# Kernel tuning notes

Measured on AMD Instinct MI355X. Metric: run time of the kernel, lower is better.

## Reference

```python
import jax, jax.numpy as jnp
import numpy as np

KERNELS = (2, 3, 6, 7)
ALPHA = 2.0
DT = 1.0  # time=1.0, step_size=1.0 -> one RK4 (3/8 rule) step, as torchdiffeq 'rk4'


def _conv(x, w, b):
    # x: [B,C,N,L], w: [O,I,1,k] -> valid conv over time axis
    y = jax.lax.conv_general_dilated(x, w, (1, 1), 'VALID',
                                     dimension_numbers=('NCHW', 'OIHW', 'NCHW'))
    return y + b[None, :, None, None]


def _inception(x, ws, bs):
    outs = [_conv(x, w, b) for w, b in zip(ws, bs)]
    L = outs[-1].shape[-1]  # shortest output (largest kernel=7)
    return jnp.concatenate([o[..., -L:] for o in outs], axis=1)


def _norm_adj(adj):
    A = adj + jnp.eye(adj.shape[0], dtype=adj.dtype)
    dinv = A.sum(1) ** -0.5
    return dinv[:, None] * A * dinv[None, :]  # D^-1/2 (A+I) D^-1/2


def _cgp(x, A_norm, mw, mb):
    f = lambda y: 0.5 * ALPHA * (jnp.einsum('ncwl,vw->ncvl', y, A_norm) - y)
    k1 = f(x)
    y2 = x + (DT / 3.0) * k1
    k2 = f(y2)
    y3 = x + DT * (k2 - k1 / 3.0)
    k3 = f(y3)
    y4 = x + DT * (k1 - k2 + k3)
    k4 = f(y4)
    yf = x + (DT / 8.0) * (k1 + 3.0 * (k2 + k3) + k4)
    # odefunc.out collects the state at each of the 4 f-evals, plus final state
    cat = jnp.concatenate([x, y2, y3, y4, yf], axis=1)  # [B, 5C, N, L]
    return _conv(cat, mw, mb)


def setup_inputs() -> dict:
    key = jax.random.key(0)
    B, C, N, T = 8, 64, 512, 64
    cq = C // 4
    ks = jax.random.split(key, 24)
    d = {
        'x': jax.random.normal(ks[0], (B, C, N, T), dtype=jnp.float32),
        'adj': jax.random.uniform(ks[1], (N, N), dtype=jnp.float32),
    }
    i = 2
    for branch in ('i1', 'i2'):
        for j, k in enumerate(KERNELS):
            d[f'{branch}w{j}'] = 0.1 * jax.random.normal(ks[i], (cq, C, 1, k), dtype=jnp.float32); i += 1
            d[f'{branch}b{j}'] = 0.1 * jax.random.normal(ks[i], (cq,), dtype=jnp.float32); i += 1
    d['m1w'] = 0.1 * jax.random.normal(ks[i], (C, 5 * C, 1, 1), dtype=jnp.float32); i += 1
    d['m1b'] = 0.1 * jax.random.normal(ks[i], (C,), dtype=jnp.float32); i += 1
    d['m2w'] = 0.1 * jax.random.normal(ks[i], (C, 5 * C, 1, 1), dtype=jnp.float32); i += 1
    d['m2b'] = 0.1 * jax.random.normal(ks[i], (C,), dtype=jnp.float32)
    return d


def reference(x, adj,
              i1w0, i1b0, i1w1, i1b1, i1w2, i1b2, i1w3, i1b3,
              i2w0, i2b0, i2w1, i2b1, i2w2, i2b2, i2w3, i2b3,
              m1w, m1b, m2w, m2b):
    T = x.shape[-1]  # receptive_field
    filt = jnp.tanh(_inception(x, (i1w0, i1w1, i1w2, i1w3), (i1b0, i1b1, i1b2, i1b3)))
    gate = jax.nn.sigmoid(_inception(x, (i2w0, i2w1, i2w2, i2w3), (i2b0, i2b1, i2b2, i2b3)))
    h = filt * gate  # dropout is identity in eval mode
    An = _norm_adj(adj)
    AnT = _norm_adj(adj.T)
    h = _cgp(h, An, m1w, m1b) + _cgp(h, AnT, m2w, m2b)
    pad = T - h.shape[-1]
    return jnp.pad(h, ((0, 0), (0, 0), (0, 0), (pad, 0)))
```

## Files before the change

kernel.cpp:

```cpp
#include <hip/hip_runtime.h>
#include <math.h>

#define NN 512
#define BB 8
#define CC 64
#define TT 64
#define LL 58
#define CL (CC*LL)
#define BCL (BB*CC*LL)
#define SZ ((size_t)NN*BCL)

typedef _Float16 half8 __attribute__((ext_vector_type(8)));
typedef _Float16 half4 __attribute__((ext_vector_type(4)));
typedef float f32x4 __attribute__((ext_vector_type(4)));

__global__ __launch_bounds__(64) void prep_adj(const float* __restrict__ adj,
                                               float* __restrict__ dinv1,
                                               float* __restrict__ dinv2){
  int v = blockIdx.x;
  int lane = threadIdx.x;
  float rs = 0.f, cs = 0.f;
  for (int w = lane; w < NN; w += 64){
    rs += adj[v*NN + w];
    cs += adj[w*NN + v];
  }
  for (int off = 32; off > 0; off >>= 1){
    rs += __shfl_down(rs, off);
    cs += __shfl_down(cs, off);
  }
  if (lane == 0){
    dinv1[v] = 1.f / sqrtf(rs + 1.f);
    dinv2[v] = 1.f / sqrtf(cs + 1.f);
  }
}

__global__ __launch_bounds__(256) void build_norm(const float* __restrict__ adj,
                                                  const float* __restrict__ dinv1,
                                                  const float* __restrict__ dinv2,
                                                  _Float16* __restrict__ An,
                                                  _Float16* __restrict__ AnT){
  int v = blockIdx.x;
  float d1v = dinv1[v], d2v = dinv2[v];
  for (int w = threadIdx.x; w < NN; w += 256){
    float diag = (v == w) ? 1.f : 0.f;
    An[v*NN + w]  = (_Float16)(d1v * (adj[v*NN + w] + diag) * dinv1[w] - diag);
    AnT[v*NN + w] = (_Float16)(d2v * (adj[w*NN + v] + diag) * dinv2[w] - diag);
  }
}

__global__ __launch_bounds__(256) void u_prep(const float* __restrict__ W1,
                                              const float* __restrict__ W2,
                                              _Float16* __restrict__ U1,
                                              _Float16* __restrict__ U2){
  const float coef[5][5] = {
    {1.f, 1.f, 1.f, 1.f, 1.f},
    {0.f, 1.f/3.f, 2.f/3.f, 1.f, 1.f},
    {0.f, 0.f, 1.f/3.f, 1.f/3.f, 0.5f},
    {0.f, 0.f, 0.f, 1.f/3.f, 1.f/6.f},
    {0.f, 0.f, 0.f, 0.f, 1.f/24.f}};
  int idx = blockIdx.x*256 + threadIdx.x;
  int o = idx / 320, rem = idx - o*320;
  int d = rem >> 6, c = rem & 63;
  float a1 = 0.f, a2 = 0.f;
  #pragma unroll
  for (int s = 0; s < 5; ++s){
    float cf = coef[d][s];
    a1 += cf * W1[o*320 + s*64 + c];
    a2 += cf * W2[o*320 + s*64 + c];
  }
  U1[idx] = (_Float16)a1;
  U2[idx] = (_Float16)a2;
}

__global__ __launch_bounds__(448) void wfg_prep(
    const float* __restrict__ w10, const float* __restrict__ w11,
    const float* __restrict__ w12, const float* __restrict__ w13,
    const float* __restrict__ w20, const float* __restrict__ w21,
    const float* __restrict__ w22, const float* __restrict__ w23,
    const float* __restrict__ b10, const float* __restrict__ b11,
    const float* __restrict__ b12, const float* __restrict__ b13,
    const float* __restrict__ b20, const float* __restrict__ b21,
    const float* __restrict__ b22, const float* __restrict__ b23,
    _Float16* __restrict__ WfG, float* __restrict__ biasFG){
  int r = blockIdx.x;
  int t = threadIdx.x;
  int qp = t >> 6, ic = t & 63;
  int gate = r >> 6;
  int j = (r >> 4) & 3;
  int oc = r & 15;
  const int kjs[4] = {2, 3, 6, 7};
  int kj = kjs[j];
  const float* wsel = gate ? ((j==0)?w20:(j==1)?w21:(j==2)?w22:w23)
                           : ((j==0)?w10:(j==1)?w11:(j==2)?w12:w13);
  int off = 7 - kj;
  float val = (qp >= off) ? wsel[(oc*64 + ic)*kj + (qp - off)] : 0.f;
  WfG[(size_t)r*448 + t] = (_Float16)val;
  if (t == 0){
    const float* bsel = gate ? ((j==0)?b20:(j==1)?b21:(j==2)?b22:b23)
                             : ((j==0)?b10:(j==1)?b11:(j==2)?b12:b13);
    biasFG[r] = bsel[oc];
  }
}

__global__ __launch_bounds__(256) void xt_prep(const float* __restrict__ x,
                                               _Float16* __restrict__ xTg){
  __shared__ float T[64][65];
  int n = blockIdx.x;
  int b = blockIdx.y;
  int tid = threadIdx.x;
  #pragma unroll
  for (int r = 0; r < 4; ++r){
    int f = tid + r*256;
    int ic = f >> 4, t4 = f & 15;
    float4 v = *(const float4*)&x[(((size_t)(b*64 + ic))*512 + n)*64 + t4*4];
    T[ic][t4*4+0] = v.x; T[ic][t4*4+1] = v.y;
    T[ic][t4*4+2] = v.z; T[ic][t4*4+3] = v.w;
  }
  __syncthreads();
  #pragma unroll
  for (int r = 0; r < 2; ++r){
    int f = tid + r*256;
    int t = f >> 3, ch = f & 7;
    half8 hv;
    #pragma unroll
    for (int q2 = 0; q2 < 8; ++q2) hv[q2] = (_Float16)T[ch*8 + q2][t];
    *(half8*)&xTg[(((size_t)(b*64 + t))*512 + n)*64 + ch*8] = hv;
  }
}

__global__ __launch_bounds__(256, 3) void inception_mfma(
    const _Float16* __restrict__ xTg,
    const _Float16* __restrict__ WfG,
    const float* __restrict__ biasFG,
    _Float16* __restrict__ S_h){
  __shared__ _Float16 X[13*32*64];
  int nt = blockIdx.x;
  int lt = blockIdx.y;
  int b  = blockIdx.z;
  int n0 = nt*32, l0 = lt*7;
  int tid = threadIdx.x;

  int sch = tid & 7, sn = (tid >> 3) & 31;
  #pragma unroll
  for (int r = 0; r < 13; ++r){
    int t = l0 + r;
    half8 v = {};
    if (t < 64)
      v = *(const half8*)&xTg[(((size_t)(b*64 + t))*512 + n0 + sn)*64 + sch*8];
    *(half8*)&X[(size_t)(r*256 + sn*8 + (sch ^ (sn & 7)))*8] = v;
  }

  int w = tid >> 6, lane = tid & 63;
  int m = lane & 15, kg = lane >> 4;

  half8 wF[14], wG[14];
  const _Float16* wb = WfG + (size_t)(w*16 + m)*448 + kg*8;
  #pragma unroll
  for (int s = 0; s < 14; ++s){
    wF[s] = *(const half8*)(wb + s*32);
    wG[s] = *(const half8*)(wb + (size_t)64*448 + s*32);
  }
  f32x4 bF = *(const f32x4*)&biasFG[w*16 + kg*4];
  f32x4 bG = *(const f32x4*)&biasFG[64 + w*16 + kg*4];

  __syncthreads();

  for (int ll = 0; ll < 7; ++ll){
    f32x4 aF0 = {}, aF1 = {}, aG0 = {}, aG1 = {};
    #pragma unroll
    for (int s = 0; s < 14; ++s){
      int t = ll + (s >> 1);
      int c0 = (s & 1)*4 + kg;
      half8 b0 = *(half8*)&X[(size_t)(t*256 + m*8        + (c0 ^ (m & 7)))*8];
      half8 b1 = *(half8*)&X[(size_t)(t*256 + (16+m)*8   + (c0 ^ (m & 7)))*8];
      aF0 = __builtin_amdgcn_mfma_f32_16x16x32_f16(wF[s], b0, aF0, 0, 0, 0);
      aG0 = __builtin_amdgcn_mfma_f32_16x16x32_f16(wG[s], b0, aG0, 0, 0, 0);
      aF1 = __builtin_amdgcn_mfma_f32_16x16x32_f16(wF[s], b1, aF1, 0, 0, 0);
      aG1 = __builtin_amdgcn_mfma_f32_16x16x32_f16(wG[s], b1, aG1, 0, 0, 0);
    }
    int l = l0 + ll;
    if (l < LL){
      #pragma unroll
      for (int rr = 0; rr < 4; ++rr){
        int c = w*16 + kg*4 + rr;
        float F0 = aF0[rr] + bF[rr];
        float G0 = aG0[rr] + bG[rr];
        float F1 = aF1[rr] + bF[rr];
        float G1 = aG1[rr] + bG[rr];
        float h0 = (2.f*__builtin_amdgcn_rcpf(1.f + __expf(-2.f*F0)) - 1.f)
                 * __builtin_amdgcn_rcpf(1.f + __expf(-G0));
        float h1 = (2.f*__builtin_amdgcn_rcpf(1.f + __expf(-2.f*F1)) - 1.f)
                 * __builtin_amdgcn_rcpf(1.f + __expf(-G1));
        size_t base = ((size_t)(b*64 + c)*LL + l)*NN + n0;
        S_h[base + m]      = (_Float16)h0;
        S_h[base + 16 + m] = (_Float16)h1;
      }
    }
  }
}

__device__ __forceinline__ void gll16(const _Float16* g, _Float16* l){
  __builtin_amdgcn_global_load_lds(
      (const __attribute__((address_space(1))) unsigned int*)g,
      (__attribute__((address_space(3))) unsigned int*)l, 16, 0, 0);
}

__global__ __launch_bounds__(512, 2) void gemm_z2(
    const _Float16* __restrict__ A0, const _Float16* __restrict__ B0,
    _Float16* __restrict__ O0,
    const _Float16* __restrict__ A1, const _Float16* __restrict__ B1,
    _Float16* __restrict__ O1){
  const _Float16* __restrict__ A = blockIdx.z ? A1 : A0;
  const _Float16* __restrict__ B = blockIdx.z ? B1 : B0;
  _Float16* __restrict__ O = blockIdx.z ? O1 : O0;

  __shared__ _Float16 L[65536];

  const int m0 = blockIdx.x * 256;
  const int v0 = blockIdx.y * 256;
  const int tid = threadIdx.x;
  const int ww = tid >> 6;
  const int lane = tid & 63;
  const int lr = lane & 15;
  const int kg = lane >> 4;
  const int wv = ww >> 2;
  const int wm = ww & 3;

  const int srow = lane >> 3;
  const int schk = (lane & 7) ^ srow;
  const _Float16* gA = A + (size_t)(v0 + ww*32 + srow)*NN + schk*8;
  const _Float16* gB = B + (size_t)(m0 + ww*32 + srow)*NN + schk*8;
  _Float16* ldsA = L + ww*2048;
  _Float16* ldsB = ldsA + 16384;

  #define STAGE(buf, kt)                                                  \
    {                                                                     \
      const _Float16* ga_ = gA + (kt)*64;                                 \
      const _Float16* gb_ = gB + (kt)*64;                                 \
      _Float16* la_ = ldsA + (buf)*32768;                                 \
      _Float16* lb_ = ldsB + (buf)*32768;                                 \
      _Pragma("unroll")                                                   \
      for (int s_ = 0; s_ < 4; ++s_){                                     \
        gll16(ga_ + (size_t)s_*8*NN, la_ + s_*512);                       \
        gll16(gb_ + (size_t)s_*8*NN, lb_ + s_*512);                       \
      }                                                                   \
    }

  f32x4 acc[8][4] = {};

  STAGE(0, 0)
  STAGE(1, 1)
  asm volatile("s_waitcnt vmcnt(8)" ::: "memory");
  asm volatile("s_barrier" ::: "memory");

  const int axor = lr & 7;
  const int aBase = (wv*128 + lr)*64;
  const int bBase = (wm*64 + lr)*64;
  const int c0 = ((kg    ) ^ axor)*8;
  const int c1 = ((kg + 4) ^ axor)*8;

  for (int kt = 0; kt < 8; ++kt){
    const _Float16* la = L + (kt & 1)*32768;
    const _Float16* lb = la + 16384;
    half8 af[8], bf[4];

    #pragma unroll
    for (int i = 0; i < 8; ++i) af[i] = *(const half8*)&la[aBase + i*1024 + c0];
    #pragma unroll
    for (int j = 0; j < 4; ++j) bf[j] = *(const half8*)&lb[bBase + j*1024 + c0];
    __builtin_amdgcn_s_setprio(1);
    #pragma unroll
    for (int i = 0; i < 8; ++i)
      #pragma unroll
      for (int j = 0; j < 4; ++j)
        acc[i][j] = __builtin_amdgcn_mfma_f32_16x16x32_f16(af[i], bf[j], acc[i][j], 0, 0, 0);
    __builtin_amdgcn_s_setprio(0);

    #pragma unroll
    for (int i = 0; i < 8; ++i) af[i] = *(const half8*)&la[aBase + i*1024 + c1];
    #pragma unroll
    for (int j = 0; j < 4; ++j) bf[j] = *(const half8*)&lb[bBase + j*1024 + c1];
    asm volatile("s_waitcnt lgkmcnt(0)" ::: "memory");
    asm volatile("s_barrier" ::: "memory");

    if (kt < 6) STAGE(kt & 1, kt + 2)

    __builtin_amdgcn_s_setprio(1);
    #pragma unroll
    for (int i = 0; i < 8; ++i)
      #pragma unroll
      for (int j = 0; j < 4; ++j)
        acc[i][j] = __builtin_amdgcn_mfma_f32_16x16x32_f16(af[i], bf[j], acc[i][j], 0, 0, 0);
    __builtin_amdgcn_s_setprio(0);

    if (kt < 6){
      asm volatile("s_waitcnt vmcnt(8)" ::: "memory");
      asm volatile("s_barrier" ::: "memory");
    } else if (kt == 6){
      asm volatile("s_waitcnt vmcnt(0)" ::: "memory");
      asm volatile("s_barrier" ::: "memory");
    }
  }
  #undef STAGE

  #pragma unroll
  for (int i = 0; i < 8; ++i){
    int vrow = v0 + wv*128 + i*16 + kg*4;
    #pragma unroll
    for (int j = 0; j < 4; ++j){
      int mcol = m0 + wm*64 + j*16 + lr;
      half4 oq;
      #pragma unroll
      for (int rr = 0; rr < 4; ++rr) oq[rr] = (_Float16)acc[i][j][rr];
      *(half4*)&O[(size_t)mcol*NN + vrow] = oq;
    }
  }
}

template<int PASS>
__global__ __launch_bounds__(256) void combine_mfma(
    const _Float16* __restrict__ Sh, const _Float16* __restrict__ S2,
    const _Float16* __restrict__ S3, const _Float16* __restrict__ S4,
    const _Float16* __restrict__ Sf,
    const _Float16* __restrict__ Wc,
    const float* __restrict__ bias,
    _Float16* __restrict__ tmp){
  __shared__ _Float16 Xsh[64*258];
  __shared__ _Float16 Wsh[64*72];
  __shared__ float Bsh[64];
  int v0 = blockIdx.x * 256;
  int l  = blockIdx.y;
  int b  = blockIdx.z;
  int tid = threadIdx.x;
  int w = tid >> 6, lane = tid & 63;
  int lr = lane & 15, kg = lane >> 4;

  if (tid < 64) Bsh[tid] = bias[tid];

  const _Float16* Sarr[5] = {Sh, S2, S3, S4, Sf};
  f32x4 acc[4][4] = {};

  for (int kt = 0; kt < 5; ++kt){
    const _Float16* S = Sarr[kt];
    __syncthreads();
    #pragma unroll
    for (int r = 0; r < 8; ++r){
      int f = tid + r*256;
      int c = f >> 5, ch = f & 31;
      half8 xv = *(const half8*)&S[((size_t)(b*64 + c)*58 + l)*512 + v0 + ch*8];
      *(half8*)&Xsh[c*258 + ch*8] = xv;
    }
    #pragma unroll
    for (int r = 0; r < 2; ++r){
      int f = tid + r*256;
      int o = f >> 3, ch = f & 7;
      *(half8*)&Wsh[o*72 + ch*8] = *(const half8*)&Wc[(size_t)o*320 + kt*64 + ch*8];
    }
    __syncthreads();

    #pragma unroll
    for (int ks = 0; ks < 2; ++ks){
      int k0 = ks*32;
      half8 aW[4];
      #pragma unroll
      for (int jj = 0; jj < 4; ++jj)
        aW[jj] = *(half8*)&Wsh[(jj*16 + lr)*72 + k0 + kg*8];
      #pragma unroll
      for (int vt = 0; vt < 4; ++vt){
        half8 bX;
        #pragma unroll
        for (int j = 0; j < 8; ++j)
          bX[j] = Xsh[(k0 + kg*8 + j)*258 + w*64 + vt*16 + lr];
        #pragma unroll
        for (int jj = 0; jj < 4; ++jj)
          acc[vt][jj] = __builtin_amdgcn_mfma_f32_16x16x32_f16(aW[jj], bX, acc[vt][jj], 0, 0, 0);
      }
    }
  }

  size_t rowbase = ((size_t)b*58 + l)*64;
  #pragma unroll
  for (int jj = 0; jj < 4; ++jj){
    #pragma unroll
    for (int rr = 0; rr < 4; ++rr){
      int o = jj*16 + kg*4 + rr;
      float bv = Bsh[o];
      size_t obase = (rowbase + o)*512 + v0 + w*64 + lr;
      #pragma unroll
      for (int vt = 0; vt < 4; ++vt){
        float val = acc[vt][jj][rr] + bv;
        size_t addr = obase + vt*16;
        if (PASS == 0) tmp[addr] = (_Float16)val;
        else           tmp[addr] = (_Float16)((float)tmp[addr] + val);
      }
    }
  }
}

__global__ __launch_bounds__(256) void untranspose(const _Float16* __restrict__ tmp,
                                                   float* __restrict__ out){
  __shared__ float T[58][65];
  int o = blockIdx.x;
  int b = blockIdx.y;
  int v0 = blockIdx.z * 64;
  int t = threadIdx.x;
  for (int idx = t; idx < 58*64; idx += 256){
    int lr = idx >> 6, vv = idx & 63;
    T[lr][vv] = (float)tmp[((size_t)(b*58 + lr)*64 + o)*NN + v0 + vv];
  }
  __syncthreads();
  #pragma unroll
  for (int i = 0; i < 16; ++i){
    int c = t + i*256;
    int vv = c >> 6, tt = c & 63;
    float val = (tt < 6) ? 0.f : T[tt - 6][vv];
    out[((size_t)(b*64 + o)*NN + v0 + vv)*TT + tt] = val;
  }
}

extern "C" void kernel_launch(void* const* d_in, const int* in_sizes, int n_in,
                              void* d_out, int out_size, void* d_ws, size_t ws_size,
                              hipStream_t stream){
  const float* x   = (const float*)d_in[0];
  const float* adj = (const float*)d_in[1];
  const float* w1[4] = {(const float*)d_in[2],  (const float*)d_in[4],
                        (const float*)d_in[6],  (const float*)d_in[8]};
  const float* b1[4] = {(const float*)d_in[3],  (const float*)d_in[5],
                        (const float*)d_in[7],  (const float*)d_in[9]};
  const float* w2[4] = {(const float*)d_in[10], (const float*)d_in[12],
                        (const float*)d_in[14], (const float*)d_in[16]};
  const float* b2[4] = {(const float*)d_in[11], (const float*)d_in[13],
                        (const float*)d_in[15], (const float*)d_in[17]};
  const float* m1w = (const float*)d_in[18];
  const float* m1b = (const float*)d_in[19];
  const float* m2w = (const float*)d_in[20];
  const float* m2b = (const float*)d_in[21];

  char* wsb = (char*)d_ws;
  float* dinv1 = (float*)(wsb);
  float* dinv2 = (float*)(wsb + 2048);
  _Float16* U1  = (_Float16*)(wsb + 4096);
  _Float16* U2  = (_Float16*)(wsb + 4096 + 40960);
  _Float16* Mn  = (_Float16*)(wsb + 167936);
  _Float16* MnT = (_Float16*)(wsb + 167936 + 524288);
  size_t sbytes = SZ * 2;
  char* sbase = wsb + 1216512;
  _Float16* S_h = (_Float16*)(sbase);
  _Float16* S2  = (_Float16*)(sbase + sbytes);
  _Float16* S3  = (_Float16*)(sbase + 2*sbytes);
  _Float16* S4  = (_Float16*)(sbase + 3*sbytes);
  _Float16* S5  = (_Float16*)(sbase + 4*sbytes);
  _Float16* tmp = (_Float16*)(sbase + 5*sbytes);
  _Float16* xTg = S2;
  _Float16* WfG = (_Float16*)(sbase + 6*sbytes);
  float* biasFG = (float*)(sbase + 6*sbytes + 114688);
  _Float16* M2  = (_Float16*)(sbase + 6*sbytes + 131072);
  _Float16* MT2 = (_Float16*)(sbase + 6*sbytes + 131072 + 524288);
  float* out = (float*)d_out;

  prep_adj<<<NN, 64, 0, stream>>>(adj, dinv1, dinv2);
  build_norm<<<NN, 256, 0, stream>>>(adj, dinv1, dinv2, Mn, MnT);
  gemm_z2<<<dim3(NN/256, NN/256, 2), 512, 0, stream>>>(MnT, Mn, M2, Mn, MnT, MT2);
  u_prep<<<80, 256, 0, stream>>>(m1w, m2w, U1, U2);
  wfg_prep<<<128, 448, 0, stream>>>(
      w1[0],w1[1],w1[2],w1[3], w2[0],w2[1],w2[2],w2[3],
      b1[0],b1[1],b1[2],b1[3], b2[0],b2[1],b2[2],b2[3], WfG, biasFG);
  xt_prep<<<dim3(NN, BB), 256, 0, stream>>>(x, xTg);
  inception_mfma<<<dim3(16, 9, 8), 256, 0, stream>>>(xTg, WfG, biasFG, S_h);

  dim3 gz(BCL/256, NN/256, 2);
  dim3 gc(2, LL, BB);
  for (int pass = 0; pass < 2; ++pass){
    const _Float16* Mp  = pass ? MnT : Mn;
    const _Float16* Mp2 = pass ? MT2 : M2;
    gemm_z2<<<gz, 512, 0, stream>>>(Mp, S_h, S2, Mp2, S_h, S3);
    gemm_z2<<<gz, 512, 0, stream>>>(Mp2, S2, S4, Mp2, S3, S5);
    if (pass == 0)
      combine_mfma<0><<<gc, 256, 0, stream>>>(S_h, S2, S3, S4, S5, U1, m1b, tmp);
    else
      combine_mfma<1><<<gc, 256, 0, stream>>>(S_h, S2, S3, S4, S5, U2, m2b, tmp);
  }
  untranspose<<<dim3(64, 8, 8), 256, 0, stream>>>(tmp, out);
}
```

Measured before the change: 529.8 us.

## Restructure gemm_z2 with half-tile pipelining, XCD-aware block remap, and LDS-staged stores

The GEMM kernel now streams each 64-wide K tile in two 32-wide halves with a new LDS swizzle, interleaving global-to-LDS prefetch with MFMA groups under finer barriers. It also flattens the grid to 1D and remaps block IDs across the 8 XCDs so that blocks sharing an operand land together. The epilogue transposes results through LDS so that global stores are coalesced 16-byte writes instead of strided half4 stores. The aim is better load/compute overlap, better L2 locality and cheaper output writes. The cost is more barriers per iteration and more complex wait-count bookkeeping.

```diff
diff --git a/kernel.cpp b/kernel.cpp
--- a/kernel.cpp
+++ b/kernel.cpp
@@ -204,20 +204,30 @@
       (const __attribute__((address_space(1))) unsigned int*)g,
       (__attribute__((address_space(3))) unsigned int*)l, 16, 0, 0);
 }
+#define BAR() asm volatile("s_barrier" ::: "memory")
 
 __global__ __launch_bounds__(512, 2) void gemm_z2(
+    int nx,
     const _Float16* __restrict__ A0, const _Float16* __restrict__ B0,
     _Float16* __restrict__ O0,
     const _Float16* __restrict__ A1, const _Float16* __restrict__ B1,
     _Float16* __restrict__ O1){
-  const _Float16* __restrict__ A = blockIdx.z ? A1 : A0;
-  const _Float16* __restrict__ B = blockIdx.z ? B1 : B0;
-  _Float16* __restrict__ O = blockIdx.z ? O1 : O0;
-
   __shared__ _Float16 L[65536];
 
-  const int m0 = blockIdx.x * 256;
-  const int v0 = blockIdx.y * 256;
+  int bid = blockIdx.x;
+  int q8 = gridDim.x >> 3;
+  int virt = (bid & 7)*q8 + (bid >> 3);
+  int y = virt & 1;
+  int pair = virt >> 1;
+  int x = pair % nx;
+  int z = pair / nx;
+
+  const _Float16* __restrict__ A = z ? A1 : A0;
+  const _Float16* __restrict__ B = z ? B1 : B0;
+  _Float16* __restrict__ O = z ? O1 : O0;
+
+  const int m0 = x * 256;
+  const int v0 = y * 256;
   const int tid = threadIdx.x;
   const int ww = tid >> 6;
   const int lane = tid & 63;
@@ -226,94 +236,110 @@
   const int wv = ww >> 2;
   const int wm = ww & 3;
 
-  const int srow = lane >> 3;
-  const int schk = (lane & 7) ^ srow;
-  const _Float16* gA = A + (size_t)(v0 + ww*32 + srow)*NN + schk*8;
-  const _Float16* gB = B + (size_t)(m0 + ww*32 + srow)*NN + schk*8;
-  _Float16* ldsA = L + ww*2048;
-  _Float16* ldsB = ldsA + 16384;
-
-  #define STAGE(buf, kt)                                                  \
-    {                                                                     \
-      const _Float16* ga_ = gA + (kt)*64;                                 \
-      const _Float16* gb_ = gB + (kt)*64;                                 \
-      _Float16* la_ = ldsA + (buf)*32768;                                 \
-      _Float16* lb_ = ldsB + (buf)*32768;                                 \
-      _Pragma("unroll")                                                   \
-      for (int s_ = 0; s_ < 4; ++s_){                                     \
-        gll16(ga_ + (size_t)s_*8*NN, la_ + s_*512);                       \
-        gll16(gb_ + (size_t)s_*8*NN, lb_ + s_*512);                       \
-      }                                                                   \
-    }
-
+  const int srow = lane >> 2;
+  const int gch  = (lane & 3) ^ (srow & 3);
+  const _Float16* gAb = A + (size_t)(v0 + ww*32 + srow)*NN + gch*8;
+  const _Float16* gBb = B + (size_t)(m0 + ww*32 + srow)*NN + gch*8;
+
+  #define STAGE_A(tt, kk)                                                   \
+    { char* l_ = (char*)L + (size_t)((tt)&1)*65536 + (size_t)(kk)*16384     \
+                 + ww*2048;                                                 \
+      const _Float16* g_ = gAb + (tt)*64 + (kk)*32;                         \
+      gll16(g_,         (_Float16*)l_);                                     \
+      gll16(g_ + 16*NN, (_Float16*)(l_ + 1024)); }
+  #define STAGE_B(tt, kk)                                                   \
+    { char* l_ = (char*)L + (size_t)((tt)&1)*65536 + 32768                  \
+                 + (size_t)(kk)*16384 + ww*2048;                            \
+      const _Float16* g_ = gBb + (tt)*64 + (kk)*32;                         \
+      gll16(g_,         (_Float16*)l_);                                     \
+      gll16(g_ + 16*NN, (_Float16*)(l_ + 1024)); }
+
+  const int csw = (kg ^ (lr & 3)) * 16;
+  const int aR = (wv*128 + lr)*64 + csw;
+  const int bR = 32768 + (wm*64 + lr)*64 + csw;
+
+  half8 af[4], bf[4];
   f32x4 acc[8][4] = {};
 
-  STAGE(0, 0)
-  STAGE(1, 1)
+  #define LOADS_A(buf, kk, ih)                                              \
+    _Pragma("unroll")                                                       \
+    for (int q_ = 0; q_ < 4; ++q_)                                          \
+      af[q_] = *(const half8*)((char*)L + (buf)*65536 + (kk)*16384          \
+                               + aR + ((ih)*4 + q_)*1024);
+  #define LOADS_B(buf, kk)                                                  \
+    _Pragma("unroll")                                                       \
+    for (int q_ = 0; q_ < 4; ++q_)                                          \
+      bf[q_] = *(const half8*)((char*)L + (buf)*65536 + (kk)*16384          \
+                               + bR + q_*1024);
+  #define MFMA16(ih)                                                        \
+    __builtin_amdgcn_s_setprio(1);                                          \
+    _Pragma("unroll")                                                       \
+    for (int i_ = 0; i_ < 4; ++i_)                                          \
+      _Pragma("unroll")                                                     \
+      for (int j_ = 0; j_ < 4; ++j_)                                        \
+        acc[(ih)*4 + i_][j_] = __builtin_amdgcn_mfma_f32_16x16x32_f16(      \
+            af[i_], bf[j_], acc[(ih)*4 + i_][j_], 0, 0, 0);                 \
+    __builtin_amdgcn_s_setprio(0);
+
+  STAGE_A(0,0) STAGE_B(0,0)
+  STAGE_A(0,1) STAGE_B(0,1)
+  STAGE_A(1,0) STAGE_B(1,0)
   asm volatile("s_waitcnt vmcnt(8)" ::: "memory");
-  asm volatile("s_barrier" ::: "memory");
-
-  const int axor = lr & 7;
-  const int aBase = (wv*128 + lr)*64;
-  const int bBase = (wm*64 + lr)*64;
-  const int c0 = ((kg    ) ^ axor)*8;
-  const int c1 = ((kg + 4) ^ axor)*8;
-
+  BAR();
+
+  #pragma unroll
   for (int kt = 0; kt < 8; ++kt){
-    const _Float16* la = L + (kt & 1)*32768;
-    const _Float16* lb = la + 16384;
-    half8 af[8], bf[4];
-
-    #pragma unroll
-    for (int i = 0; i < 8; ++i) af[i] = *(const half8*)&la[aBase + i*1024 + c0];
-    #pragma unroll
-    for (int j = 0; j < 4; ++j) bf[j] = *(const half8*)&lb[bBase + j*1024 + c0];
-    __builtin_amdgcn_s_setprio(1);
-    #pragma unroll
-    for (int i = 0; i < 8; ++i)
-      #pragma unroll
-      for (int j = 0; j < 4; ++j)
-        acc[i][j] = __builtin_amdgcn_mfma_f32_16x16x32_f16(af[i], bf[j], acc[i][j], 0, 0, 0);
-    __builtin_amdgcn_s_setprio(0);
-
-    #pragma unroll
-    for (int i = 0; i < 8; ++i) af[i] = *(const half8*)&la[aBase + i*1024 + c1];
-    #pragma unroll
-    for (int j = 0; j < 4; ++j) bf[j] = *(const half8*)&lb[bBase + j*1024 + c1];
-    asm volatile("s_waitcnt lgkmcnt(0)" ::: "memory");
-    asm volatile("s_barrier" ::: "memory");
-
-    if (kt < 6) STAGE(kt & 1, kt + 2)
-
-    __builtin_amdgcn_s_setprio(1);
-    #pragma unroll
-    for (int i = 0; i < 8; ++i)
-      #pragma unroll
-      for (int j = 0; j < 4; ++j)
-        acc[i][j] = __builtin_amdgcn_mfma_f32_16x16x32_f16(af[i], bf[j], acc[i][j], 0, 0, 0);
-    __builtin_amdgcn_s_setprio(0);
-
-    if (kt < 6){
-      asm volatile("s_waitcnt vmcnt(8)" ::: "memory");
-      asm volatile("s_barrier" ::: "memory");
-    } else if (kt == 6){
-      asm volatile("s_waitcnt vmcnt(0)" ::: "memory");
-      asm volatile("s_barrier" ::: "memory");
-    }
-  }
-  #undef STAGE
-
-  #pragma unroll
-  for (int i = 0; i < 8; ++i){
-    int vrow = v0 + wv*128 + i*16 + kg*4;
-    #pragma unroll
-    for (int j = 0; j < 4; ++j){
-      int mcol = m0 + wm*64 + j*16 + lr;
+    const int buf = kt & 1;
+    LOADS_A(buf, 0, 0); LOADS_B(buf, 0);
+    if (kt + 1 < 8) STAGE_A(kt+1, 1)
+    BAR();
+    MFMA16(0);
+    BAR();
+    LOADS_A(buf, 0, 1);
+    if (kt + 1 < 8) STAGE_B(kt+1, 1)
+    BAR();
+    MFMA16(1);
+    if (kt < 7) { asm volatile("s_waitcnt vmcnt(8)" ::: "memory"); }
+    else        { asm volatile("s_waitcnt vmcnt(0)" ::: "memory"); }
+    BAR();
+    LOADS_A(buf, 1, 0); LOADS_B(buf, 1);
+    if (kt + 2 < 8) STAGE_A(kt+2, 0)
+    BAR();
+    MFMA16(0);
+    BAR();
+    LOADS_A(buf, 1, 1);
+    if (kt + 2 < 8) STAGE_B(kt+2, 0)
+    BAR();
+    MFMA16(1);
+    if (kt < 6)      { asm volatile("s_waitcnt vmcnt(8)" ::: "memory"); }
+    else if (kt == 6){ asm volatile("s_waitcnt vmcnt(4)" ::: "memory"); }
+    BAR();
+  }
+  #undef STAGE_A
+  #undef STAGE_B
+  #undef LOADS_A
+  #undef LOADS_B
+  #undef MFMA16
+
+  char* Lw = (char*)L + ww*16384;
+  #pragma unroll
+  for (int j = 0; j < 4; ++j){
+    int row = j*16 + lr;
+    #pragma unroll
+    for (int i = 0; i < 8; ++i){
+      int c = (i*4 + kg) ^ ((lr & 7)*4);
       half4 oq;
       #pragma unroll
       for (int rr = 0; rr < 4; ++rr) oq[rr] = (_Float16)acc[i][j][rr];
-      *(half4*)&O[(size_t)mcol*NN + vrow] = oq;
-    }
+      *(half4*)(Lw + row*256 + c*8) = oq;
+    }
+  }
+  #pragma unroll
+  for (int s = 0; s < 16; ++s){
+    int row = s*4 + kg;
+    int cc = (2*lr) ^ ((row & 7)*4);
+    half8 hv = *(const half8*)(Lw + row*256 + cc*8);
+    *(half8*)&O[(size_t)(m0 + wm*64 + row)*NN + v0 + wv*128 + lr*8] = hv;
   }
 }
 
@@ -460,7 +486,7 @@
 
   prep_adj<<<NN, 64, 0, stream>>>(adj, dinv1, dinv2);
   build_norm<<<NN, 256, 0, stream>>>(adj, dinv1, dinv2, Mn, MnT);
-  gemm_z2<<<dim3(NN/256, NN/256, 2), 512, 0, stream>>>(MnT, Mn, M2, Mn, MnT, MT2);
+  gemm_z2<<<8, 512, 0, stream>>>(2, MnT, Mn, M2, Mn, MnT, MT2);
   u_prep<<<80, 256, 0, stream>>>(m1w, m2w, U1, U2);
   wfg_prep<<<128, 448, 0, stream>>>(
       w1[0],w1[1],w1[2],w1[3], w2[0],w2[1],w2[2],w2[3],
@@ -468,13 +494,12 @@
   xt_prep<<<dim3(NN, BB), 256, 0, stream>>>(x, xTg);
   inception_mfma<<<dim3(16, 9, 8), 256, 0, stream>>>(xTg, WfG, biasFG, S_h);
 
-  dim3 gz(BCL/256, NN/256, 2);
   dim3 gc(2, LL, BB);
   for (int pass = 0; pass < 2; ++pass){
     const _Float16* Mp  = pass ? MnT : Mn;
     const _Float16* Mp2 = pass ? MT2 : M2;
-    gemm_z2<<<gz, 512, 0, stream>>>(Mp, S_h, S2, Mp2, S_h, S3);
-    gemm_z2<<<gz, 512, 0, stream>>>(Mp2, S2, S4, Mp2, S3, S5);
+    gemm_z2<<<464, 512, 0, stream>>>(116, Mp, S_h, S2, Mp2, S_h, S3);
+    gemm_z2<<<464, 512, 0, stream>>>(116, Mp2, S2, S4, Mp2, S3, S5);
     if (pass == 0)
       combine_mfma<0><<<gc, 256, 0, stream>>>(S_h, S2, S3, S4, S5, U1, m1b, tmp);
     else
```

After: 491.7 us. 7.2% less time.
